# Optimization experiments

Measured on AMD Instinct MI355X. Metric: run time of the kernel, lower is better.

## Reference

```python
import jax, jax.numpy as jnp
import numpy as np

H, C = 8, 8  # num_heads, c_hidden; c_m = H*C = 64
LN_EPS = 1e-5


def setup_inputs() -> dict:
    key = jax.random.key(0)
    ks = jax.random.split(key, 8)
    B, S, L, CM = 2, 512, 384, H * C
    m = jax.random.normal(ks[0], (B, S, L, CM), dtype=jnp.float32)
    msa_mask = jax.random.randint(ks[1], (B, S, L), 0, 2).astype(jnp.float32)
    sc = 1.0 / np.sqrt(CM)
    return {
        "m": m,
        "msa_mask": msa_mask,
        "ln_w": jnp.ones((CM,), jnp.float32),
        "ln_b": jnp.zeros((CM,), jnp.float32),
        "wq": jax.random.normal(ks[2], (CM, H * C), jnp.float32) * sc,
        "wk": jax.random.normal(ks[3], (CM, H * C), jnp.float32) * sc,
        "wv": jax.random.normal(ks[4], (CM, H * C), jnp.float32) * sc,
        "wg": jax.random.normal(ks[5], (CM, H * C), jnp.float32) * sc,
        "bg": jnp.ones((H * C,), jnp.float32),
        "wo": jax.random.normal(ks[6], (H * C, CM), jnp.float32) * sc,
        "bo": jnp.zeros((CM,), jnp.float32),
    }


def reference(m, msa_mask, ln_w, ln_b, wq, wk, wv, wg, bg, wo, bo):
    B, S, L, CM = m.shape
    # LayerNorm over c_m
    mu = jnp.mean(m, axis=-1, keepdims=True)
    var = jnp.mean(jnp.square(m - mu), axis=-1, keepdims=True)
    x = (m - mu) * jax.lax.rsqrt(var + LN_EPS) * ln_w + ln_b

    k = (x @ wk).reshape(B, S, L, H, C)
    v = (x @ wv).reshape(B, S, L, H, C)
    g = jax.nn.sigmoid(x @ wg + bg).reshape(B, S, L, H, C)

    # masked mean over the sequence axis S -> global query per residue
    denom = jnp.maximum(jnp.sum(msa_mask, axis=1), 1.0)  # [B, L]
    q_input = jnp.sum(x * msa_mask[..., None], axis=1) / denom[..., None]  # [B, L, CM]
    q = (q_input @ wq).reshape(B, L, H, C)

    logits = jnp.einsum("blhc,bslhc->blhs", q, k) / np.sqrt(C).astype(np.float32)
    mask_bls = jnp.transpose(msa_mask, (0, 2, 1))[:, :, None, :]  # [B, L, 1, S]
    logits = jnp.where(mask_bls == 0, -1e9, logits)
    attn = jax.nn.softmax(logits, axis=-1)  # [B, L, H, S]

    out_global = jnp.einsum("blhs,bslhc->blhc", attn, v)  # [B, L, H, C]
    out = g * out_global[:, None]  # broadcast over S -> [B, S, L, H, C]
    out = out.reshape(B, S, L, H * C) @ wo + bo
    out = out * msa_mask[..., None]
    return out
```

## Files before the change

kernel.cpp:

```cpp
#include <hip/hip_runtime.h>

#define NH 8
#define DCM 64
#define NB 2
#define NS 512
#define NL 384
#define LN_EPS 1e-5f
#define INV_SQRT_C 0.35355339059327379f

typedef __attribute__((ext_vector_type(8))) short short8v;
typedef __attribute__((ext_vector_type(4))) float f32x4;

__device__ __forceinline__ float4 ld4(const float* p) {
  return *reinterpret_cast<const float4*>(p);
}
__device__ __forceinline__ unsigned short f2bf(float f) {
  unsigned int b = __float_as_uint(f);
  b += 0x7FFFu + ((b >> 16) & 1u);
  return (unsigned short)(b >> 16);
}
__device__ __forceinline__ float bf2f(unsigned short u) {
  return __uint_as_float(((unsigned int)u) << 16);
}

__global__ void prep_weights(const float* __restrict__ wg,
                             const float* __restrict__ wo,
                             const float* __restrict__ wv,
                             unsigned short* __restrict__ wt) {
  int i = blockIdx.x * 256 + threadIdx.x;
  if (i < 4096) {
    int n = i >> 6, k = i & 63;
    wt[i]        = f2bf(wg[k * DCM + n]);
    wt[4096 + i] = f2bf(wo[k * DCM + n]);
    wt[8192 + i] = f2bf(wv[k * DCM + n]);
  }
}

__global__ __launch_bounds__(256) void fused(
    const float* __restrict__ m, const float* __restrict__ msk,
    const float* __restrict__ lnw, const float* __restrict__ lnb,
    const float* __restrict__ wq, const float* __restrict__ wk,
    const unsigned short* __restrict__ wt,
    const float* __restrict__ bg, const float* __restrict__ bo,
    float* __restrict__ out)
{
  const int col = blockIdx.x;
  const int b = col / NL, l = col % NL;
  const int tid = threadIdx.x;
  const int wave = tid >> 6, lane = tid & 63;

  __shared__ __align__(16) unsigned short x_lds[NS * DCM];
  __shared__ __align__(16) unsigned short mask_s[NS];
  __shared__ __align__(16) unsigned char scratch[8192];
  __shared__ __align__(16) unsigned short qk_bf[16 * DCM];
  __shared__ float smred[4][8];
  __shared__ __align__(16) float ogred[4][DCM];
  __shared__ float og_s[DCM];

  float* redf = (float*)scratch;
  float* dredf = redf + 256;
  float* qinf = redf + 272;
  float* qsf  = redf + 336;
  unsigned short* P_T = (unsigned short*)scratch;
  unsigned short* a2t = (unsigned short*)scratch;

  for (int i = tid; i < NS; i += 256)
    mask_s[i] = f2bf(msk[(b * NS + i) * NL + l]);

  const int c8 = lane & 7;
  const int r8 = lane >> 3;
  float lw8[8], lb8[8];
#pragma unroll
  for (int k = 0; k < 8; ++k) { lw8[k] = lnw[c8 * 8 + k]; lb8[k] = lnb[c8 * 8 + k]; }
  __syncthreads();

  float qacc[8] = {0.f,0.f,0.f,0.f,0.f,0.f,0.f,0.f};
  float dacc = 0.f;
  const int rowbase = wave * 128;
  {
    const size_t rstep = (size_t)8 * NL * DCM;
    const float* mb = m + ((size_t)b * NS * NL + l) * DCM + c8 * 8
                    + (size_t)(rowbase + r8) * NL * DCM;
    auto process = [&](const float4& A, const float4& Bv, int s) {
      float xv[8] = {A.x, A.y, A.z, A.w, Bv.x, Bv.y, Bv.z, Bv.w};
      float s1 = 0.f, s2 = 0.f;
#pragma unroll
      for (int k = 0; k < 8; ++k) { s1 += xv[k]; s2 += xv[k] * xv[k]; }
#pragma unroll
      for (int o = 1; o <= 4; o <<= 1) { s1 += __shfl_xor(s1, o); s2 += __shfl_xor(s2, o); }
      const float mu = s1 * 0.015625f;
      const float rs = rsqrtf(s2 * 0.015625f - mu * mu + LN_EPS);
      const float mk = bf2f(mask_s[s]);
      short8v xp;
#pragma unroll
      for (int k = 0; k < 8; ++k) {
        float xn = (xv[k] - mu) * rs * lw8[k] + lb8[k];
        xp[k] = (short)f2bf(xn);
        qacc[k] += xn * mk;
      }
      dacc += mk;
      *reinterpret_cast<short8v*>(&x_lds[s * DCM + ((c8 * 8) ^ ((s & 7) << 3))]) = xp;
    };
    float4 f0a = ld4(mb),             f0b = ld4(mb + 4);
    float4 f1a = ld4(mb + rstep),     f1b = ld4(mb + rstep + 4);
    float4 f2a = ld4(mb + 2 * rstep), f2b = ld4(mb + 2 * rstep + 4);
    float4 f3a = ld4(mb + 3 * rstep), f3b = ld4(mb + 3 * rstep + 4);
#pragma unroll
    for (int blk = 0; blk < 4; ++blk) {
      const int it0 = blk * 4;
      process(f0a, f0b, rowbase + (it0 + 0) * 8 + r8);
      if (blk < 3) { f0a = ld4(mb + (size_t)(it0 + 4) * rstep);
                     f0b = ld4(mb + (size_t)(it0 + 4) * rstep + 4); }
      process(f1a, f1b, rowbase + (it0 + 1) * 8 + r8);
      if (blk < 3) { f1a = ld4(mb + (size_t)(it0 + 5) * rstep);
                     f1b = ld4(mb + (size_t)(it0 + 5) * rstep + 4); }
      process(f2a, f2b, rowbase + (it0 + 2) * 8 + r8);
      if (blk < 3) { f2a = ld4(mb + (size_t)(it0 + 6) * rstep);
                     f2b = ld4(mb + (size_t)(it0 + 6) * rstep + 4); }
      process(f3a, f3b, rowbase + (it0 + 3) * 8 + r8);
      if (blk < 3) { f3a = ld4(mb + (size_t)(it0 + 7) * rstep);
                     f3b = ld4(mb + (size_t)(it0 + 7) * rstep + 4); }
    }
  }
#pragma unroll
  for (int o = 8; o <= 32; o <<= 1) {
#pragma unroll
    for (int k = 0; k < 8; ++k) qacc[k] += __shfl_xor(qacc[k], o);
    dacc += __shfl_xor(dacc, o);
  }
  if (lane < 8) {
    float4 t0; t0.x = qacc[0]; t0.y = qacc[1]; t0.z = qacc[2]; t0.w = qacc[3];
    float4 t1; t1.x = qacc[4]; t1.y = qacc[5]; t1.z = qacc[6]; t1.w = qacc[7];
    *reinterpret_cast<float4*>(&redf[wave * DCM + lane * 8])     = t0;
    *reinterpret_cast<float4*>(&redf[wave * DCM + lane * 8 + 4]) = t1;
  }
  if (lane == 0) dredf[wave] = dacc;
  __syncthreads();

  if (tid < DCM) {
    float dn = fmaxf(dredf[0] + dredf[1] + dredf[2] + dredf[3], 1.0f);
    qinf[tid] = (redf[tid] + redf[DCM + tid] + redf[2 * DCM + tid] + redf[3 * DCM + tid]) / dn;
  }
  __syncthreads();
  if (tid < DCM) {
    float a = 0.f;
    for (int j = 0; j < DCM; ++j) a += qinf[j] * wq[j * DCM + tid];
    qsf[tid] = a;
  }
  __syncthreads();
  for (int idx = tid; idx < 16 * DCM; idx += 256) {
    int h = idx >> 6, cm = idx & 63;
    float a = 0.f;
    if (h < NH) {
#pragma unroll
      for (int c = 0; c < 8; ++c) a += qsf[h * 8 + c] * wk[cm * DCM + h * 8 + c];
      a *= INV_SQRT_C;
    }
    qk_bf[idx] = f2bf(a);
  }
  __syncthreads();

  const int bcol = lane & 15;
  const int kg = lane >> 4;
  short8v qkB0 = *reinterpret_cast<const short8v*>(&qk_bf[bcol * DCM + kg * 8]);
  short8v qkB1 = *reinterpret_cast<const short8v*>(&qk_bf[bcol * DCM + 32 + kg * 8]);
  float smacc = 0.f;
  for (int t = 0; t < 8; ++t) {
    const int arow = wave * 128 + t * 16 + bcol;
    const int swz = (arow & 7) << 3;
    short8v a0 = *reinterpret_cast<const short8v*>(&x_lds[arow * DCM + ((kg * 8) ^ swz)]);
    short8v a1 = *reinterpret_cast<const short8v*>(&x_lds[arow * DCM + ((32 + kg * 8) ^ swz)]);
    f32x4 L = (f32x4){0.f, 0.f, 0.f, 0.f};
    L = __builtin_amdgcn_mfma_f32_16x16x32_bf16(a0, qkB0, L, 0, 0, 0);
    L = __builtin_amdgcn_mfma_f32_16x16x32_bf16(a1, qkB1, L, 0, 0, 0);
    const int s0 = wave * 128 + t * 16 + kg * 4;
    short4 mk4 = *reinterpret_cast<const short4*>(&mask_s[s0]);
    float p0 = bf2f((unsigned short)mk4.x) * __expf(L[0]);
    float p1 = bf2f((unsigned short)mk4.y) * __expf(L[1]);
    float p2 = bf2f((unsigned short)mk4.z) * __expf(L[2]);
    float p3 = bf2f((unsigned short)mk4.w) * __expf(L[3]);
    smacc += (p0 + p1) + (p2 + p3);
    if (bcol < NH) {
      short4 pw;
      pw.x = (short)f2bf(p0); pw.y = (short)f2bf(p1);
      pw.z = (short)f2bf(p2); pw.w = (short)f2bf(p3);
      *reinterpret_cast<short4*>(&P_T[bcol * NS + (s0 ^ (bcol << 3))]) = pw;
    }
  }
  smacc += __shfl_xor(smacc, 16); smacc += __shfl_xor(smacc, 32);
  if (lane < NH) smred[wave][lane] = smacc;
  __syncthreads();

  short8v wvB[4][2];
#pragma unroll
  for (int nt = 0; nt < 4; ++nt)
#pragma unroll
    for (int kw = 0; kw < 2; ++kw)
      wvB[nt][kw] = *reinterpret_cast<const short8v*>(
          &wt[8192 + (nt * 16 + bcol) * DCM + kw * 32 + kg * 8]);
  float ogacc[4] = {0.f, 0.f, 0.f, 0.f};
  for (int t = 0; t < 8; ++t) {
    const int arow = wave * 128 + t * 16 + bcol;
    const int swz = (arow & 7) << 3;
    short8v a0 = *reinterpret_cast<const short8v*>(&x_lds[arow * DCM + ((kg * 8) ^ swz)]);
    short8v a1 = *reinterpret_cast<const short8v*>(&x_lds[arow * DCM + ((32 + kg * 8) ^ swz)]);
    const int s0 = wave * 128 + t * 16 + kg * 4;
#pragma unroll
    for (int nt = 0; nt < 4; ++nt) {
      f32x4 V = (f32x4){0.f, 0.f, 0.f, 0.f};
      V = __builtin_amdgcn_mfma_f32_16x16x32_bf16(a0, wvB[nt][0], V, 0, 0, 0);
      V = __builtin_amdgcn_mfma_f32_16x16x32_bf16(a1, wvB[nt][1], V, 0, 0, 0);
      const int h2 = 2 * nt + (bcol >> 3);
      short4 p4 = *reinterpret_cast<const short4*>(&P_T[h2 * NS + (s0 ^ (h2 << 3))]);
      ogacc[nt] += bf2f((unsigned short)p4.x) * V[0]
                 + bf2f((unsigned short)p4.y) * V[1]
                 + bf2f((unsigned short)p4.z) * V[2]
                 + bf2f((unsigned short)p4.w) * V[3];
    }
  }
#pragma unroll
  for (int nt = 0; nt < 4; ++nt) {
    ogacc[nt] += __shfl_xor(ogacc[nt], 16);
    ogacc[nt] += __shfl_xor(ogacc[nt], 32);
  }
  if (lane < 16) {
#pragma unroll
    for (int nt = 0; nt < 4; ++nt) ogred[wave][nt * 16 + lane] = ogacc[nt];
  }
  __syncthreads();
  if (tid < DCM) {
    float smT = fmaxf(smred[0][tid >> 3] + smred[1][tid >> 3]
                    + smred[2][tid >> 3] + smred[3][tid >> 3], 1e-30f);
    og_s[tid] = (ogred[0][tid] + ogred[1][tid] + ogred[2][tid] + ogred[3][tid]) / smT;
  }
  __syncthreads();

  short8v wgB[4][2], woB[4][2];
  float bgv[4], bov[4], ogv[4];
#pragma unroll
  for (int nt = 0; nt < 4; ++nt) {
    const int ncol = nt * 16 + bcol;
#pragma unroll
    for (int kw = 0; kw < 2; ++kw) {
      wgB[nt][kw] = *reinterpret_cast<const short8v*>(&wt[ncol * DCM + kw * 32 + kg * 8]);
      woB[nt][kw] = *reinterpret_cast<const short8v*>(&wt[4096 + ncol * DCM + kw * 32 + kg * 8]);
    }
    bgv[nt] = bg[ncol]; bov[nt] = bo[ncol]; ogv[nt] = og_s[ncol];
  }
  const size_t outbase = ((size_t)b * NS * NL + l) * DCM;
  unsigned short* a2w = &a2t[wave * 16 * DCM];

  for (int t = 0; t < 8; ++t) {
    const int arow = wave * 128 + t * 16 + bcol;
    const int swz = (arow & 7) << 3;
    short8v a0 = *reinterpret_cast<const short8v*>(&x_lds[arow * DCM + ((kg * 8) ^ swz)]);
    short8v a1 = *reinterpret_cast<const short8v*>(&x_lds[arow * DCM + ((32 + kg * 8) ^ swz)]);
    f32x4 accG[4];
#pragma unroll
    for (int nt = 0; nt < 4; ++nt) {
      accG[nt] = (f32x4){0.f, 0.f, 0.f, 0.f};
      accG[nt] = __builtin_amdgcn_mfma_f32_16x16x32_bf16(a0, wgB[nt][0], accG[nt], 0, 0, 0);
      accG[nt] = __builtin_amdgcn_mfma_f32_16x16x32_bf16(a1, wgB[nt][1], accG[nt], 0, 0, 0);
    }
#pragma unroll
    for (int nt = 0; nt < 4; ++nt) {
      const int cc = nt * 16 + bcol;
#pragma unroll
      for (int r = 0; r < 4; ++r) {
        const int r2 = kg * 4 + r;
        float gx = accG[nt][r] + bgv[nt];
        float g = 1.0f / (1.0f + __expf(-gx));
        a2w[r2 * DCM + (cc ^ ((r2 & 7) << 3))] = f2bf(g * ogv[nt]);
      }
    }
    short8v b0 = *reinterpret_cast<const short8v*>(
        &a2w[bcol * DCM + ((kg * 8) ^ ((bcol & 7) << 3))]);
    short8v b1 = *reinterpret_cast<const short8v*>(
        &a2w[bcol * DCM + ((32 + kg * 8) ^ ((bcol & 7) << 3))]);
    f32x4 accO[4];
#pragma unroll
    for (int nt = 0; nt < 4; ++nt) {
      accO[nt] = (f32x4){0.f, 0.f, 0.f, 0.f};
      accO[nt] = __builtin_amdgcn_mfma_f32_16x16x32_bf16(b0, woB[nt][0], accO[nt], 0, 0, 0);
      accO[nt] = __builtin_amdgcn_mfma_f32_16x16x32_bf16(b1, woB[nt][1], accO[nt], 0, 0, 0);
    }
#pragma unroll
    for (int nt = 0; nt < 4; ++nt) {
#pragma unroll
      for (int r = 0; r < 4; ++r) {
        const int orow = wave * 128 + t * 16 + kg * 4 + r;
        const float mk = bf2f(mask_s[orow]);
        out[outbase + (size_t)orow * NL * DCM + nt * 16 + bcol] = (accO[nt][r] + bov[nt]) * mk;
      }
    }
  }
}

extern "C" void kernel_launch(void* const* d_in, const int* in_sizes, int n_in,
                              void* d_out, int out_size, void* d_ws, size_t ws_size,
                              hipStream_t stream) {
  (void)in_sizes; (void)n_in; (void)out_size; (void)ws_size;
  const float* m   = (const float*)d_in[0];
  const float* msk = (const float*)d_in[1];
  const float* lnw = (const float*)d_in[2];
  const float* lnb = (const float*)d_in[3];
  const float* wq  = (const float*)d_in[4];
  const float* wk  = (const float*)d_in[5];
  const float* wv  = (const float*)d_in[6];
  const float* wg  = (const float*)d_in[7];
  const float* bg  = (const float*)d_in[8];
  const float* wo  = (const float*)d_in[9];
  const float* bo  = (const float*)d_in[10];
  unsigned short* wt = (unsigned short*)d_ws;
  float* out = (float*)d_out;

  prep_weights<<<dim3(16), dim3(256), 0, stream>>>(wg, wo, wv, wt);
  fused<<<dim3(NB * NL), dim3(256), 0, stream>>>(
      m, msk, lnw, lnb, wq, wk, wt, bg, bo, out);
}
```

Before: 69.93 us.

## Use 512 threads per block, fuse logits and V passes, reuse x_lds for gated output

Doubles the block to 8 waves so each wave handles 64 sequence rows instead of 128, raising per-CU parallelism while keeping 768 blocks. The softmax-logit pass and the V-projection pass are merged into one loop over tiles, which drops an intermediate barrier and a second read of x_lds. The gated intermediate is now written in place over each wave's own x_lds rows instead of a separate scratch buffer. Register pressure under launch_bounds(512,4) and the bigger scratch region may limit occupancy.

```diff
diff --git a/kernel.cpp b/kernel.cpp
--- a/kernel.cpp
+++ b/kernel.cpp
@@ -36,7 +36,7 @@
   }
 }
 
-__global__ __launch_bounds__(256) void fused(
+__global__ __launch_bounds__(512, 4) void fused(
     const float* __restrict__ m, const float* __restrict__ msk,
     const float* __restrict__ lnw, const float* __restrict__ lnb,
     const float* __restrict__ wq, const float* __restrict__ wk,
@@ -51,20 +51,19 @@
 
   __shared__ __align__(16) unsigned short x_lds[NS * DCM];
   __shared__ __align__(16) unsigned short mask_s[NS];
-  __shared__ __align__(16) unsigned char scratch[8192];
+  __shared__ __align__(16) unsigned char scratch[10752];
   __shared__ __align__(16) unsigned short qk_bf[16 * DCM];
-  __shared__ float smred[4][8];
-  __shared__ __align__(16) float ogred[4][DCM];
-  __shared__ float og_s[DCM];
-
-  float* redf = (float*)scratch;
-  float* dredf = redf + 256;
-  float* qinf = redf + 272;
-  float* qsf  = redf + 336;
+
+  float* redf  = (float*)scratch;
+  float* dredf = redf + 512;
+  float* qinf  = redf + 528;
+  float* qsf   = redf + 592;
   unsigned short* P_T = (unsigned short*)scratch;
-  unsigned short* a2t = (unsigned short*)scratch;
-
-  for (int i = tid; i < NS; i += 256)
+  float* ogredf = (float*)(scratch + 8192);
+  float* smredf = (float*)(scratch + 10240);
+  float* ogsf   = (float*)(scratch + 10496);
+
+  for (int i = tid; i < NS; i += 512)
     mask_s[i] = f2bf(msk[(b * NS + i) * NL + l]);
 
   const int c8 = lane & 7;
@@ -76,7 +75,7 @@
 
   float qacc[8] = {0.f,0.f,0.f,0.f,0.f,0.f,0.f,0.f};
   float dacc = 0.f;
-  const int rowbase = wave * 128;
+  const int rowbase = wave * 64;
   {
     const size_t rstep = (size_t)8 * NL * DCM;
     const float* mb = m + ((size_t)b * NS * NL + l) * DCM + c8 * 8
@@ -106,19 +105,19 @@
     float4 f2a = ld4(mb + 2 * rstep), f2b = ld4(mb + 2 * rstep + 4);
     float4 f3a = ld4(mb + 3 * rstep), f3b = ld4(mb + 3 * rstep + 4);
 #pragma unroll
-    for (int blk = 0; blk < 4; ++blk) {
+    for (int blk = 0; blk < 2; ++blk) {
       const int it0 = blk * 4;
       process(f0a, f0b, rowbase + (it0 + 0) * 8 + r8);
-      if (blk < 3) { f0a = ld4(mb + (size_t)(it0 + 4) * rstep);
+      if (blk < 1) { f0a = ld4(mb + (size_t)(it0 + 4) * rstep);
                      f0b = ld4(mb + (size_t)(it0 + 4) * rstep + 4); }
       process(f1a, f1b, rowbase + (it0 + 1) * 8 + r8);
-      if (blk < 3) { f1a = ld4(mb + (size_t)(it0 + 5) * rstep);
+      if (blk < 1) { f1a = ld4(mb + (size_t)(it0 + 5) * rstep);
                      f1b = ld4(mb + (size_t)(it0 + 5) * rstep + 4); }
       process(f2a, f2b, rowbase + (it0 + 2) * 8 + r8);
-      if (blk < 3) { f2a = ld4(mb + (size_t)(it0 + 6) * rstep);
+      if (blk < 1) { f2a = ld4(mb + (size_t)(it0 + 6) * rstep);
                      f2b = ld4(mb + (size_t)(it0 + 6) * rstep + 4); }
       process(f3a, f3b, rowbase + (it0 + 3) * 8 + r8);
-      if (blk < 3) { f3a = ld4(mb + (size_t)(it0 + 7) * rstep);
+      if (blk < 1) { f3a = ld4(mb + (size_t)(it0 + 7) * rstep);
                      f3b = ld4(mb + (size_t)(it0 + 7) * rstep + 4); }
     }
   }
@@ -138,8 +137,10 @@
   __syncthreads();
 
   if (tid < DCM) {
-    float dn = fmaxf(dredf[0] + dredf[1] + dredf[2] + dredf[3], 1.0f);
-    qinf[tid] = (redf[tid] + redf[DCM + tid] + redf[2 * DCM + tid] + redf[3 * DCM + tid]) / dn;
+    float dn = 0.f, a = 0.f;
+#pragma unroll
+    for (int w = 0; w < 8; ++w) { dn += dredf[w]; a += redf[w * DCM + tid]; }
+    qinf[tid] = a / fmaxf(dn, 1.0f);
   }
   __syncthreads();
   if (tid < DCM) {
@@ -148,7 +149,7 @@
     qsf[tid] = a;
   }
   __syncthreads();
-  for (int idx = tid; idx < 16 * DCM; idx += 256) {
+  for (int idx = tid; idx < 16 * DCM; idx += 512) {
     int h = idx >> 6, cm = idx & 63;
     float a = 0.f;
     if (h < NH) {
@@ -164,16 +165,25 @@
   const int kg = lane >> 4;
   short8v qkB0 = *reinterpret_cast<const short8v*>(&qk_bf[bcol * DCM + kg * 8]);
   short8v qkB1 = *reinterpret_cast<const short8v*>(&qk_bf[bcol * DCM + 32 + kg * 8]);
+  short8v wvB[4][2];
+#pragma unroll
+  for (int nt = 0; nt < 4; ++nt)
+#pragma unroll
+    for (int kw = 0; kw < 2; ++kw)
+      wvB[nt][kw] = *reinterpret_cast<const short8v*>(
+          &wt[8192 + (nt * 16 + bcol) * DCM + kw * 32 + kg * 8]);
   float smacc = 0.f;
-  for (int t = 0; t < 8; ++t) {
-    const int arow = wave * 128 + t * 16 + bcol;
+  float ogacc[4] = {0.f, 0.f, 0.f, 0.f};
+  for (int t = 0; t < 4; ++t) {
+    const int tilebase = rowbase + t * 16;
+    const int arow = tilebase + bcol;
     const int swz = (arow & 7) << 3;
     short8v a0 = *reinterpret_cast<const short8v*>(&x_lds[arow * DCM + ((kg * 8) ^ swz)]);
     short8v a1 = *reinterpret_cast<const short8v*>(&x_lds[arow * DCM + ((32 + kg * 8) ^ swz)]);
     f32x4 L = (f32x4){0.f, 0.f, 0.f, 0.f};
     L = __builtin_amdgcn_mfma_f32_16x16x32_bf16(a0, qkB0, L, 0, 0, 0);
     L = __builtin_amdgcn_mfma_f32_16x16x32_bf16(a1, qkB1, L, 0, 0, 0);
-    const int s0 = wave * 128 + t * 16 + kg * 4;
+    const int s0 = tilebase + kg * 4;
     short4 mk4 = *reinterpret_cast<const short4*>(&mask_s[s0]);
     float p0 = bf2f((unsigned short)mk4.x) * __expf(L[0]);
     float p1 = bf2f((unsigned short)mk4.y) * __expf(L[1]);
@@ -186,38 +196,25 @@
       pw.z = (short)f2bf(p2); pw.w = (short)f2bf(p3);
       *reinterpret_cast<short4*>(&P_T[bcol * NS + (s0 ^ (bcol << 3))]) = pw;
     }
-  }
-  smacc += __shfl_xor(smacc, 16); smacc += __shfl_xor(smacc, 32);
-  if (lane < NH) smred[wave][lane] = smacc;
-  __syncthreads();
-
-  short8v wvB[4][2];
-#pragma unroll
-  for (int nt = 0; nt < 4; ++nt)
-#pragma unroll
-    for (int kw = 0; kw < 2; ++kw)
-      wvB[nt][kw] = *reinterpret_cast<const short8v*>(
-          &wt[8192 + (nt * 16 + bcol) * DCM + kw * 32 + kg * 8]);
-  float ogacc[4] = {0.f, 0.f, 0.f, 0.f};
-  for (int t = 0; t < 8; ++t) {
-    const int arow = wave * 128 + t * 16 + bcol;
-    const int swz = (arow & 7) << 3;
-    short8v a0 = *reinterpret_cast<const short8v*>(&x_lds[arow * DCM + ((kg * 8) ^ swz)]);
-    short8v a1 = *reinterpret_cast<const short8v*>(&x_lds[arow * DCM + ((32 + kg * 8) ^ swz)]);
-    const int s0 = wave * 128 + t * 16 + kg * 4;
-#pragma unroll
-    for (int nt = 0; nt < 4; ++nt) {
-      f32x4 V = (f32x4){0.f, 0.f, 0.f, 0.f};
-      V = __builtin_amdgcn_mfma_f32_16x16x32_bf16(a0, wvB[nt][0], V, 0, 0, 0);
-      V = __builtin_amdgcn_mfma_f32_16x16x32_bf16(a1, wvB[nt][1], V, 0, 0, 0);
+    f32x4 V[4];
+#pragma unroll
+    for (int nt = 0; nt < 4; ++nt) {
+      V[nt] = (f32x4){0.f, 0.f, 0.f, 0.f};
+      V[nt] = __builtin_amdgcn_mfma_f32_16x16x32_bf16(a0, wvB[nt][0], V[nt], 0, 0, 0);
+      V[nt] = __builtin_amdgcn_mfma_f32_16x16x32_bf16(a1, wvB[nt][1], V[nt], 0, 0, 0);
+    }
+#pragma unroll
+    for (int nt = 0; nt < 4; ++nt) {
       const int h2 = 2 * nt + (bcol >> 3);
       short4 p4 = *reinterpret_cast<const short4*>(&P_T[h2 * NS + (s0 ^ (h2 << 3))]);
-      ogacc[nt] += bf2f((unsigned short)p4.x) * V[0]
-                 + bf2f((unsigned short)p4.y) * V[1]
-                 + bf2f((unsigned short)p4.z) * V[2]
-                 + bf2f((unsigned short)p4.w) * V[3];
-    }
-  }
+      ogacc[nt] += bf2f((unsigned short)p4.x) * V[nt][0]
+                 + bf2f((unsigned short)p4.y) * V[nt][1]
+                 + bf2f((unsigned short)p4.z) * V[nt][2]
+                 + bf2f((unsigned short)p4.w) * V[nt][3];
+    }
+  }
+  smacc += __shfl_xor(smacc, 16); smacc += __shfl_xor(smacc, 32);
+  if (lane < NH) smredf[wave * NH + lane] = smacc;
 #pragma unroll
   for (int nt = 0; nt < 4; ++nt) {
     ogacc[nt] += __shfl_xor(ogacc[nt], 16);
@@ -225,13 +222,17 @@
   }
   if (lane < 16) {
 #pragma unroll
-    for (int nt = 0; nt < 4; ++nt) ogred[wave][nt * 16 + lane] = ogacc[nt];
+    for (int nt = 0; nt < 4; ++nt) ogredf[wave * DCM + nt * 16 + lane] = ogacc[nt];
   }
   __syncthreads();
   if (tid < DCM) {
-    float smT = fmaxf(smred[0][tid >> 3] + smred[1][tid >> 3]
-                    + smred[2][tid >> 3] + smred[3][tid >> 3], 1e-30f);
-    og_s[tid] = (ogred[0][tid] + ogred[1][tid] + ogred[2][tid] + ogred[3][tid]) / smT;
+    float smT = 0.f, a = 0.f;
+#pragma unroll
+    for (int w = 0; w < 8; ++w) {
+      smT += smredf[w * NH + (tid >> 3)];
+      a += ogredf[w * DCM + tid];
+    }
+    ogsf[tid] = a / fmaxf(smT, 1e-30f);
   }
   __syncthreads();
 
@@ -245,13 +246,13 @@
       wgB[nt][kw] = *reinterpret_cast<const short8v*>(&wt[ncol * DCM + kw * 32 + kg * 8]);
       woB[nt][kw] = *reinterpret_cast<const short8v*>(&wt[4096 + ncol * DCM + kw * 32 + kg * 8]);
     }
-    bgv[nt] = bg[ncol]; bov[nt] = bo[ncol]; ogv[nt] = og_s[ncol];
+    bgv[nt] = bg[ncol]; bov[nt] = bo[ncol]; ogv[nt] = ogsf[ncol];
   }
   const size_t outbase = ((size_t)b * NS * NL + l) * DCM;
-  unsigned short* a2w = &a2t[wave * 16 * DCM];
-
-  for (int t = 0; t < 8; ++t) {
-    const int arow = wave * 128 + t * 16 + bcol;
+
+  for (int t = 0; t < 4; ++t) {
+    const int tilebase = rowbase + t * 16;
+    const int arow = tilebase + bcol;
     const int swz = (arow & 7) << 3;
     short8v a0 = *reinterpret_cast<const short8v*>(&x_lds[arow * DCM + ((kg * 8) ^ swz)]);
     short8v a1 = *reinterpret_cast<const short8v*>(&x_lds[arow * DCM + ((32 + kg * 8) ^ swz)]);
@@ -270,13 +271,13 @@
         const int r2 = kg * 4 + r;
         float gx = accG[nt][r] + bgv[nt];
         float g = 1.0f / (1.0f + __expf(-gx));
-        a2w[r2 * DCM + (cc ^ ((r2 & 7) << 3))] = f2bf(g * ogv[nt]);
+        x_lds[(tilebase + r2) * DCM + (cc ^ ((r2 & 7) << 3))] = f2bf(g * ogv[nt]);
       }
     }
     short8v b0 = *reinterpret_cast<const short8v*>(
-        &a2w[bcol * DCM + ((kg * 8) ^ ((bcol & 7) << 3))]);
+        &x_lds[(tilebase + bcol) * DCM + ((kg * 8) ^ ((bcol & 7) << 3))]);
     short8v b1 = *reinterpret_cast<const short8v*>(
-        &a2w[bcol * DCM + ((32 + kg * 8) ^ ((bcol & 7) << 3))]);
+        &x_lds[(tilebase + bcol) * DCM + ((32 + kg * 8) ^ ((bcol & 7) << 3))]);
     f32x4 accO[4];
 #pragma unroll
     for (int nt = 0; nt < 4; ++nt) {
@@ -288,7 +289,7 @@
     for (int nt = 0; nt < 4; ++nt) {
 #pragma unroll
       for (int r = 0; r < 4; ++r) {
-        const int orow = wave * 128 + t * 16 + kg * 4 + r;
+        const int orow = tilebase + kg * 4 + r;
         const float mk = bf2f(mask_s[orow]);
         out[outbase + (size_t)orow * NL * DCM + nt * 16 + bcol] = (accO[nt][r] + bov[nt]) * mk;
       }
@@ -315,6 +316,6 @@
   float* out = (float*)d_out;
 
   prep_weights<<<dim3(16), dim3(256), 0, stream>>>(wg, wo, wv, wt);
-  fused<<<dim3(NB * NL), dim3(256), 0, stream>>>(
+  fused<<<dim3(NB * NL), dim3(512), 0, stream>>>(
       m, msk, lnw, lnb, wq, wk, wt, bg, bo, out);
 }
```

After: 84.59 us. 1.21x slower.
